# Performance work log

Hardware: AMD Instinct MI355X
Metric: run time of the kernel (lower is better)

## Reference

```python
import jax, jax.numpy as jnp
import numpy as np

VOCAB, EMBED, HIDDEN, NCLS, PAD = 50257, 512, 1024, 2, 0

def setup_inputs() -> dict:
    key = jax.random.key(0)
    ks = jax.random.split(key, 16)
    def xavier(k, shape):
        fan_in, fan_out = shape[1], shape[0]
        lim = jnp.sqrt(6.0 / (fan_in + fan_out))
        return jax.random.uniform(k, shape, jnp.float32, -lim, lim)
    x = jax.random.randint(ks[0], (64, 512), 0, VOCAB, dtype=jnp.int32)
    emb = jax.random.uniform(ks[1], (VOCAB, EMBED), jnp.float32, -0.1, 0.1)
    emb = emb.at[PAD].set(0.0)
    return {
        'x': x,
        'emb': emb,
        'W_ii': xavier(ks[2], (HIDDEN, EMBED)), 'b_ii': jnp.zeros((HIDDEN,), jnp.float32),
        'W_hi': xavier(ks[3], (HIDDEN, HIDDEN)),
        'W_if': xavier(ks[4], (HIDDEN, EMBED)), 'b_if': jnp.zeros((HIDDEN,), jnp.float32),
        'W_hf': xavier(ks[5], (HIDDEN, HIDDEN)),
        'W_ig': xavier(ks[6], (HIDDEN, EMBED)), 'b_ig': jnp.zeros((HIDDEN,), jnp.float32),
        'W_hg': xavier(ks[7], (HIDDEN, HIDDEN)),
        'W_io': xavier(ks[8], (HIDDEN, EMBED)), 'b_io': jnp.zeros((HIDDEN,), jnp.float32),
        'W_ho': xavier(ks[9], (HIDDEN, HIDDEN)),
        'V_w': xavier(ks[10], (NCLS, HIDDEN)), 'V_b': jnp.zeros((NCLS,), jnp.float32),
    }


def _lstm_forward(x, emb, W_ii, b_ii, W_hi, W_if, b_if, W_hf, W_ig, b_ig, W_hg, W_io, b_io, W_ho, V_w, V_b):
    # Dropout layers act as identity in eval mode.
    e = emb[x]  # [B,S,E]
    B, S, E = e.shape
    H = W_hi.shape[0]
    # Precompute all input-to-gate projections in one batched GEMM.
    Wx = jnp.stack([W_ii, W_if, W_ig, W_io], axis=0)      # [4,H,E]
    bx = jnp.stack([b_ii, b_if, b_ig, b_io], axis=0)      # [4,H]
    gates_x = jnp.einsum('bse,ghe->sbgh', e, Wx) + bx     # [S,B,4,H]
    Wh = jnp.stack([W_hi, W_hf, W_hg, W_ho], axis=0)      # [4,H,H]

    def step(carry, gx):
        h, c = carry
        gh = jnp.einsum('bk,ghk->bgh', h, Wh)             # [B,4,H]
        g = gx + gh
        i_t = jax.nn.sigmoid(g[:, 0])
        f_t = jax.nn.sigmoid(g[:, 1])
        g_t = jnp.tanh(g[:, 2])
        o_t = jax.nn.sigmoid(g[:, 3])
        c = f_t * c + i_t * g_t
        h = o_t * jnp.tanh(c)
        return (h, c), None

    h0 = jnp.zeros((B, H), e.dtype)
    c0 = jnp.zeros((B, H), e.dtype)
    (h, c), _ = jax.lax.scan(step, (h0, c0), gates_x)
    out = h @ V_w.T + V_b
    return out, (h, c)


def reference(x, emb, W_ii, b_ii, W_hi, W_if, b_if, W_hf, W_ig, b_ig, W_hg, W_io, b_io, W_ho, V_w, V_b):
    return _lstm_forward(x, emb, W_ii, b_ii, W_hi, W_if, b_if, W_hf, W_ig, b_ig, W_hg, W_io, b_io, W_ho, V_w, V_b)
```

## Files before the change

### kernel.cpp

```cpp
#include <hip/hip_runtime.h>
#include <math.h>

#define Bn 64
#define Hn 1024
#define En 512
#define Sn 512
#define RING 32
#define NBLK 256

typedef _Float16 f16;
typedef _Float16 half8 __attribute__((ext_vector_type(8)));
typedef float f32x4 __attribute__((ext_vector_type(4)));
typedef unsigned long long u64;
typedef u64 u64x2 __attribute__((ext_vector_type(2)));


__global__ __launch_bounds__(256) void wpack_kernel(
    const float* __restrict__ Whi_, const float* __restrict__ Whf_,
    const float* __restrict__ Whg_, const float* __restrict__ Who_,
    const float* __restrict__ Wxi_, const float* __restrict__ Wxf_,
    const float* __restrict__ Wxg_, const float* __restrict__ Wxo_,
    f16* __restrict__ wpHi, f16* __restrict__ wpLo)
{
    int t = blockIdx.x * 256 + threadIdx.x;
    int lane = t & 63;
    int rest = t >> 6;
    int kc = rest % 48;
    int bb = rest / 48;
    int n = lane & 15, g = n >> 2, du = n & 3;
    int u = bb * 4 + du;
    int klo = (lane >> 4) << 3;
    const float* Wh = (g == 0 ? Whi_ : g == 1 ? Whf_ : g == 2 ? Whg_ : Who_);
    const float* Wx = (g == 0 ? Wxi_ : g == 1 ? Wxf_ : g == 2 ? Wxg_ : Wxo_);
    const float* src = (kc < 32) ? (Wh + (size_t)u * Hn + kc * 32 + klo)
                                 : (Wx + (size_t)u * En + (kc - 32) * 32 + klo);
    float4 v0 = ((const float4*)src)[0];
    float4 v1 = ((const float4*)src)[1];
    float w[8] = {v0.x, v0.y, v0.z, v0.w, v1.x, v1.y, v1.z, v1.w};
    #pragma unroll
    for (int j = 0; j < 8; ++j) {
        f16 hi = (f16)w[j];
        float lo = (w[j] - (float)hi) * 2048.0f;
        wpHi[(size_t)t * 8 + j] = hi;
        wpLo[(size_t)t * 8 + j] = (f16)lo;
    }
}

__global__ __launch_bounds__(256) void epack_kernel(
    const int* __restrict__ x, const float* __restrict__ emb,
    f16* __restrict__ eF)
{
    int t = blockIdx.x * 256 + threadIdx.x;
    int lane = t & 63;
    int q = t >> 6;
    int mt = q & 3; q >>= 2;
    int kc2 = q & 15;
    int s = q >> 4;
    int b = mt * 16 + (lane & 15);
    int tok = x[b * Sn + s];
    int k = kc2 * 32 + ((lane >> 4) << 3);
    const float* src = emb + (size_t)tok * En + k;
    float4 v0 = ((const float4*)src)[0];
    float4 v1 = ((const float4*)src)[1];
    f16* dst = eF + (size_t)t * 8;
    dst[0] = (f16)v0.x; dst[1] = (f16)v0.y; dst[2] = (f16)v0.z; dst[3] = (f16)v0.w;
    dst[4] = (f16)v1.x; dst[5] = (f16)v1.y; dst[6] = (f16)v1.z; dst[7] = (f16)v1.w;
}

__global__ __launch_bounds__(256) void gx_chunk_kernel(
    const half8* __restrict__ eF,
    const half8* __restrict__ wpHi, const half8* __restrict__ wpLo,
    float* __restrict__ gx, int chunk)
{
    int lane = threadIdx.x & 63;
    int id = blockIdx.x * 4 + (threadIdx.x >> 6);
    int sc = id >> 8;
    int bb = id & 255;
    int s = chunk * RING + sc;

    const half8* eFs = eF + (size_t)s * 4096 + lane;
    const half8* bH = wpHi + ((size_t)(bb * 48 + 32)) * 64 + lane;
    const half8* bL = wpLo + ((size_t)(bb * 48 + 32)) * 64 + lane;

    f32x4 aH[4], aL[4];
    #pragma unroll
    for (int mt = 0; mt < 4; ++mt) { aH[mt] = (f32x4)0.0f; aL[mt] = (f32x4)0.0f; }

    for (int kcx = 0; kcx < 16; ++kcx) {
        half8 bh = bH[(size_t)kcx * 64];
        half8 bl = bL[(size_t)kcx * 64];
        #pragma unroll
        for (int mt = 0; mt < 4; ++mt) {
            half8 a = eFs[(size_t)((kcx * 4 + mt) * 64)];
            aH[mt] = __builtin_amdgcn_mfma_f32_16x16x32_f16(a, bh, aH[mt], 0, 0, 0);
            aL[mt] = __builtin_amdgcn_mfma_f32_16x16x32_f16(a, bl, aL[mt], 0, 0, 0);
        }
    }

    int n = lane & 15, g = n >> 2, du = n & 3;
    int col = (g << 10) + bb * 4 + du;
    float* g0 = gx + (size_t)sc * (Bn * 4096) + col;
    #pragma unroll
    for (int mt = 0; mt < 4; ++mt) {
        #pragma unroll
        for (int r = 0; r < 4; ++r) {
            int b = mt * 16 + ((lane >> 4) << 2) + r;
            g0[(size_t)b * 4096] = aH[mt][r] + aL[mt][r] * (1.0f / 2048.0f);
        }
    }
}

template<bool USE_GX>
__global__ __launch_bounds__(1024) void step_kernel(
    const f16* __restrict__ hFin, f16* __restrict__ hFout,
    const half8* __restrict__ eF,
    const half8* __restrict__ wpHi, const half8* __restrict__ wpLo,
    const float* __restrict__ gx,
    const float* __restrict__ bi, const float* __restrict__ bf,
    const float* __restrict__ bg, const float* __restrict__ bo,
    float* __restrict__ c, float* __restrict__ hFinal, int s)
{
    __shared__ float preW[16][256];

    const int tid  = threadIdx.x;
    const int lane = tid & 63;
    const int wv   = tid >> 6;
    const int mt   = wv & 3;
    const int kq   = wv >> 2;
    const int bb   = blockIdx.x;

    const half8* hin = (const half8*)hFin + lane;
    const half8* bHb = wpHi + (size_t)(bb * 48) * 64 + lane;
    const half8* bLb = wpLo + (size_t)(bb * 48) * 64 + lane;

    f32x4 accH = {0.f, 0.f, 0.f, 0.f};
    f32x4 accL = {0.f, 0.f, 0.f, 0.f};

    if (USE_GX) {
        #pragma unroll
        for (int i = 0; i < 8; ++i) {
            int kc = kq * 8 + i;
            half8 a  = hin[(size_t)((kc * 4 + mt) * 64)];
            half8 bh = bHb[(size_t)kc * 64];
            half8 bl = bLb[(size_t)kc * 64];
            accH = __builtin_amdgcn_mfma_f32_16x16x32_f16(a, bh, accH, 0, 0, 0);
            accL = __builtin_amdgcn_mfma_f32_16x16x32_f16(a, bl, accL, 0, 0, 0);
        }
    } else {
        const half8* eFs = eF + (size_t)s * 4096 + lane;
        #pragma unroll
        for (int i = 0; i < 12; ++i) {
            int kc = kq * 12 + i;
            half8 a = (kc < 32) ? hin[(size_t)((kc * 4 + mt) * 64)]
                                : eFs[(size_t)(((kc - 32) * 4 + mt) * 64)];
            half8 bh = bHb[(size_t)kc * 64];
            half8 bl = bLb[(size_t)kc * 64];
            accH = __builtin_amdgcn_mfma_f32_16x16x32_f16(a, bh, accH, 0, 0, 0);
            accL = __builtin_amdgcn_mfma_f32_16x16x32_f16(a, bl, accL, 0, 0, 0);
        }
    }

    f32x4 v;
    #pragma unroll
    for (int r = 0; r < 4; ++r) v[r] = accH[r] + accL[r] * (1.0f / 2048.0f);
    *(f32x4*)&preW[wv][lane * 4] = v;
    __syncthreads();

    if (tid < 256) {
        const int bcell = tid >> 2, ducell = tid & 3;
        const int colcell = bb * 4 + ducell;
        const int msub = bcell & 15, mtp = bcell >> 4;
        const int base_i = ((msub >> 2) * 16) * 4 + (msub & 3);
        float sg_[4];
        #pragma unroll
        for (int g = 0; g < 4; ++g) {
            int idx = base_i + (g * 4 + ducell) * 4;
            sg_[g] = preW[0 * 4 + mtp][idx] + preW[1 * 4 + mtp][idx]
                   + preW[2 * 4 + mtp][idx] + preW[3 * 4 + mtp][idx];
        }
        float si = sg_[0] + bi[colcell];
        float sf = sg_[1] + bf[colcell];
        float sg = sg_[2] + bg[colcell];
        float so = sg_[3] + bo[colcell];
        if (USE_GX) {
            const float* gr = gx + ((size_t)(s & (RING - 1)) * Bn + bcell) * 4096;
            si += gr[colcell];        sf += gr[1024 + colcell];
            sg += gr[2048 + colcell]; so += gr[3072 + colcell];
        }
        float it = 1.f / (1.f + expf(-si));
        float ft = 1.f / (1.f + expf(-sf));
        float gt = tanhf(sg);
        float ot = 1.f / (1.f + expf(-so));
        int gi = bcell * Hn + colcell;
        float cn = ft * c[gi] + it * gt;
        c[gi] = cn;
        float hn = ot * tanhf(cn);
        int kch = colcell >> 5, dk = colcell & 31;
        int lp  = ((dk >> 3) << 4) | (bcell & 15);
        int mtp2 = bcell >> 4;
        hFout[((size_t)((kch * 4 + mtp2) * 64 + lp)) * 8 + (dk & 7)] = (f16)hn;
        if (s == Sn - 1) hFinal[gi] = hn;
    }
}

__global__ __launch_bounds__(1024) void steps_chunk_coop(
    f16* __restrict__ hF,
    const half8* __restrict__ eF,
    const half8* __restrict__ wpHi, const half8* __restrict__ wpLo,
    float* __restrict__ gx,
    const float* __restrict__ bi, const float* __restrict__ bf,
    const float* __restrict__ bg, const float* __restrict__ bo,
    float* __restrict__ c, float* __restrict__ hFinal,
    unsigned* __restrict__ cntArr, int chunk)
{
    __shared__ alignas(16) f16 wHs[32 * 512];
    __shared__ alignas(16) f16 wLs[32 * 512];
    __shared__ float preW[16][256];

    const int tid  = threadIdx.x;
    const int lane = tid & 63;
    const int wv   = tid >> 6;
    const int mt   = wv & 3;
    const int kq   = wv >> 2;
    const int bb   = blockIdx.x;

    {
        const half8* srcH = wpHi + (size_t)(bb * 48) * 64;
        const half8* srcL = wpLo + (size_t)(bb * 48) * 64;
        half8* dH = (half8*)wHs;
        half8* dL = (half8*)wLs;
        #pragma unroll
        for (int i = 0; i < 2; ++i) {
            dH[tid + i * 1024] = srcH[tid + i * 1024];
            dL[tid + i * 1024] = srcL[tid + i * 1024];
        }
    }

    {
        const half8* bH = wpHi + ((size_t)(bb * 48 + 32)) * 64 + lane;
        const half8* bL = wpLo + ((size_t)(bb * 48 + 32)) * 64 + lane;
        #pragma unroll
        for (int t2 = 0; t2 < 2; ++t2) {
            int sc = wv * 2 + t2;
            int s = chunk * RING + sc;
            const half8* eFs = eF + (size_t)s * 4096 + lane;
            f32x4 aH[4], aL[4];
            #pragma unroll
            for (int m2 = 0; m2 < 4; ++m2) { aH[m2] = (f32x4)0.0f; aL[m2] = (f32x4)0.0f; }
            for (int kcx = 0; kcx < 16; ++kcx) {
                half8 bh = bH[(size_t)kcx * 64];
                half8 bl = bL[(size_t)kcx * 64];
                #pragma unroll
                for (int m2 = 0; m2 < 4; ++m2) {
                    half8 a = eFs[(size_t)((kcx * 4 + m2) * 64)];
                    aH[m2] = __builtin_amdgcn_mfma_f32_16x16x32_f16(a, bh, aH[m2], 0, 0, 0);
                    aL[m2] = __builtin_amdgcn_mfma_f32_16x16x32_f16(a, bl, aL[m2], 0, 0, 0);
                }
            }
            int n = lane & 15, g = n >> 2, du = n & 3;
            int col = (g << 10) + bb * 4 + du;
            float* g0 = gx + (size_t)sc * (Bn * 4096) + col;
            #pragma unroll
            for (int m2 = 0; m2 < 4; ++m2) {
                #pragma unroll
                for (int r = 0; r < 4; ++r) {
                    int b = m2 * 16 + ((lane >> 4) << 2) + r;
                    g0[(size_t)b * 4096] = aH[m2][r] + aL[m2][r] * (1.0f / 2048.0f);
                }
            }
        }
    }

    float creg = 0.f, bi_r = 0.f, bf_r = 0.f, bg_r = 0.f, bo_r = 0.f;
    int bcell = 0, ducell = 0, colcell = 0, gi = 0, mtp = 0, base_i = 0;
    int kch = 0, dk = 0, lp = 0;
    if (tid < 256) {
        bcell = tid >> 2; ducell = tid & 3;
        colcell = bb * 4 + ducell;
        gi = bcell * Hn + colcell;
        int msub = bcell & 15; mtp = bcell >> 4;
        base_i = ((msub >> 2) * 16) * 4 + (msub & 3);
        creg = c[gi];
        bi_r = bi[colcell]; bf_r = bf[colcell];
        bg_r = bg[colcell]; bo_r = bo[colcell];
        kch = colcell >> 5; dk = colcell & 31;
        lp  = ((dk >> 3) << 4) | (bcell & 15);
    }

    __syncthreads();

    const half8* wHl = (const half8*)wHs + lane;
    const half8* wLl = (const half8*)wLs + lane;

    #pragma unroll 1
    for (int sc = 0; sc < RING; ++sc) {
        const int s = chunk * RING + sc;
        const f16* hbase = hF + (size_t)(s & 1) * 65536;
        f16* hout = hF + (size_t)((s + 1) & 1) * 65536;

        float gxi = 0.f, gxf = 0.f, gxg = 0.f, gxo = 0.f;
        if (tid < 256) {
            const float* gr = gx + ((size_t)sc * Bn + bcell) * 4096 + colcell;
            gxi = gr[0];    gxf = gr[1024];
            gxg = gr[2048]; gxo = gr[3072];
        }

        half8 afr[8];
        #pragma unroll
        for (int i = 0; i < 8; ++i) {
            const int kc = kq * 8 + i;
            const u64* p = (const u64*)(hbase
                + ((size_t)((kc * 4 + mt) * 64 + lane)) * 8);
            u64x2 u;
            u.x = __hip_atomic_load(p, __ATOMIC_RELAXED,
                                    __HIP_MEMORY_SCOPE_AGENT);
            u.y = __hip_atomic_load(p + 1, __ATOMIC_RELAXED,
                                    __HIP_MEMORY_SCOPE_AGENT);
            afr[i] = __builtin_bit_cast(half8, u);
        }

        f32x4 accH = {0.f, 0.f, 0.f, 0.f};
        f32x4 accL = {0.f, 0.f, 0.f, 0.f};
        #pragma unroll
        for (int i = 0; i < 8; ++i) {
            const int kc = kq * 8 + i;
            half8 bh = wHl[(size_t)kc * 64];
            half8 bl = wLl[(size_t)kc * 64];
            accH = __builtin_amdgcn_mfma_f32_16x16x32_f16(afr[i], bh, accH, 0, 0, 0);
            accL = __builtin_amdgcn_mfma_f32_16x16x32_f16(afr[i], bl, accL, 0, 0, 0);
        }
        f32x4 v;
        #pragma unroll
        for (int r = 0; r < 4; ++r) v[r] = accH[r] + accL[r] * (1.0f / 2048.0f);
        *(f32x4*)&preW[wv][lane * 4] = v;
        __syncthreads();

        if (tid < 256) {
            float sg_[4];
            #pragma unroll
            for (int g = 0; g < 4; ++g) {
                int idx = base_i + (g * 4 + ducell) * 4;
                sg_[g] = preW[mtp][idx] + preW[4 + mtp][idx]
                       + preW[8 + mtp][idx] + preW[12 + mtp][idx];
            }
            float si = sg_[0] + bi_r + gxi;
            float sf = sg_[1] + bf_r + gxf;
            float sg = sg_[2] + bg_r + gxg;
            float so = sg_[3] + bo_r + gxo;
            float it = 1.f / (1.f + expf(-si));
            float ft = 1.f / (1.f + expf(-sf));
            float gt = tanhf(sg);
            float ot = 1.f / (1.f + expf(-so));
            float cn = ft * creg + it * gt;
            creg = cn;
            float hn = ot * tanhf(cn);
            union { f16 h; unsigned short u; } cv;
            cv.h = (f16)hn;
            unsigned short* paddr = (unsigned short*)(hout
                + ((size_t)((kch * 4 + mtp) * 64 + lp)) * 8 + (dk & 7));
            __hip_atomic_store(paddr, cv.u, __ATOMIC_RELAXED,
                               __HIP_MEMORY_SCOPE_AGENT);
            if (s == Sn - 1) hFinal[gi] = hn;
        }

        if (sc < RING - 1) {
            asm volatile("s_waitcnt vmcnt(0)" ::: "memory");
            __syncthreads();
            if (tid == 0) {
                const unsigned B = (unsigned)(chunk * (RING - 1) + sc);
                unsigned old = __hip_atomic_fetch_add(
                    cntArr + ((unsigned)(bb & 15) << 5), 1u,
                    __ATOMIC_RELAXED, __HIP_MEMORY_SCOPE_AGENT);
                if ((old & 15u) == 15u) {
                    unsigned m = __hip_atomic_fetch_add(
                        cntArr + 512, 1u,
                        __ATOMIC_RELAXED, __HIP_MEMORY_SCOPE_AGENT);
                    if (m == 16u * B + 15u)
                        __hip_atomic_store(cntArr + 544, B + 1u,
                            __ATOMIC_RELAXED, __HIP_MEMORY_SCOPE_AGENT);
                }
                while (__hip_atomic_load(cntArr + 544, __ATOMIC_RELAXED,
                                         __HIP_MEMORY_SCOPE_AGENT) < B + 1u)
                    __builtin_amdgcn_s_sleep(1);
            }
            __syncthreads();
        }
    }

    if (tid < 256) c[gi] = creg;
}

__global__ __launch_bounds__(256) void copy_hc(
    const float* __restrict__ h, const float* __restrict__ c,
    float* __restrict__ out)
{
    int i = blockIdx.x * 256 + threadIdx.x;
    out[128 + i] = h[i];
    out[128 + Bn * Hn + i] = c[i];
}

__global__ __launch_bounds__(64) void classifier(
    const float* __restrict__ h, const float* __restrict__ Vw,
    const float* __restrict__ Vb, float* __restrict__ out)
{
    int bid = blockIdx.x;
    int b = bid >> 1, n = bid & 1;
    int lane = threadIdx.x;
    float sum = 0.f;
    for (int k = lane; k < Hn; k += 64)
        sum += h[b * Hn + k] * Vw[n * Hn + k];
    #pragma unroll
    for (int off = 32; off > 0; off >>= 1)
        sum += __shfl_down(sum, off, 64);
    if (lane == 0)
        out[b * 2 + n] = sum + Vb[n];
}


#define KT 128
#define KTP 132

__global__ __launch_bounds__(256) void lstm_step_fb(
    const int* __restrict__ x, const float* __restrict__ emb,
    const float* __restrict__ Wxi, const float* __restrict__ Wxf,
    const float* __restrict__ Wxg, const float* __restrict__ Wxo,
    const float* __restrict__ bi, const float* __restrict__ bf,
    const float* __restrict__ bg, const float* __restrict__ bo,
    const float* __restrict__ Whi, const float* __restrict__ Whf,
    const float* __restrict__ Whg, const float* __restrict__ Who,
    const float* __restrict__ h_in, const float* __restrict__ c_in,
    float* __restrict__ h_out, float* __restrict__ c_out, int s)
{
    __shared__ float sh[Bn][KTP];
    __shared__ float sw[16][KTP];
    const int tid = threadIdx.x;
    const int b = tid >> 2, j = tid & 3;
    const int cb = blockIdx.x * 4, col = cb + j;
    float acc0 = 0.f, acc1 = 0.f, acc2 = 0.f, acc3 = 0.f;

    for (int k0 = 0; k0 < En; k0 += KT) {
        for (int i = tid; i < Bn * (KT / 4); i += 256) {
            int bl = i >> 5, k4 = (i & 31) << 2;
            int tok = x[bl * Sn + s];
            *reinterpret_cast<float4*>(&sh[bl][k4]) =
                *reinterpret_cast<const float4*>(&emb[(size_t)tok * En + k0 + k4]);
        }
        for (int i = tid; i < 16 * (KT / 4); i += 256) {
            int r = i >> 5, k4 = (i & 31) << 2;
            const float* Wg = (r < 8) ? ((r < 4) ? Wxi : Wxf)
                                      : ((r < 12) ? Wxg : Wxo);
            *reinterpret_cast<float4*>(&sw[r][k4]) =
                *reinterpret_cast<const float4*>(&Wg[(size_t)(cb + (r & 3)) * En + k0 + k4]);
        }
        __syncthreads();
        #pragma unroll 8
        for (int k = 0; k < KT; k += 4) {
            float4 hv = *reinterpret_cast<const float4*>(&sh[b][k]);
            float4 w0 = *reinterpret_cast<const float4*>(&sw[j][k]);
            float4 w1 = *reinterpret_cast<const float4*>(&sw[4 + j][k]);
            float4 w2 = *reinterpret_cast<const float4*>(&sw[8 + j][k]);
            float4 w3 = *reinterpret_cast<const float4*>(&sw[12 + j][k]);
            acc0 += hv.x*w0.x + hv.y*w0.y + hv.z*w0.z + hv.w*w0.w;
            acc1 += hv.x*w1.x + hv.y*w1.y + hv.z*w1.z + hv.w*w1.w;
            acc2 += hv.x*w2.x + hv.y*w2.y + hv.z*w2.z + hv.w*w2.w;
            acc3 += hv.x*w3.x + hv.y*w3.y + hv.z*w3.z + hv.w*w3.w;
        }
        __syncthreads();
    }
    for (int k0 = 0; k0 < Hn; k0 += KT) {
        for (int i = tid; i < Bn * (KT / 4); i += 256) {
            int bl = i >> 5, k4 = (i & 31) << 2;
            *reinterpret_cast<float4*>(&sh[bl][k4]) =
                *reinterpret_cast<const float4*>(&h_in[(size_t)bl * Hn + k0 + k4]);
        }
        for (int i = tid; i < 16 * (KT / 4); i += 256) {
            int r = i >> 5, k4 = (i & 31) << 2;
            const float* Wg = (r < 8) ? ((r < 4) ? Whi : Whf)
                                      : ((r < 12) ? Whg : Who);
            *reinterpret_cast<float4*>(&sw[r][k4]) =
                *reinterpret_cast<const float4*>(&Wg[(size_t)(cb + (r & 3)) * Hn + k0 + k4]);
        }
        __syncthreads();
        #pragma unroll 8
        for (int k = 0; k < KT; k += 4) {
            float4 hv = *reinterpret_cast<const float4*>(&sh[b][k]);
            float4 w0 = *reinterpret_cast<const float4*>(&sw[j][k]);
            float4 w1 = *reinterpret_cast<const float4*>(&sw[4 + j][k]);
            float4 w2 = *reinterpret_cast<const float4*>(&sw[8 + j][k]);
            float4 w3 = *reinterpret_cast<const float4*>(&sw[12 + j][k]);
            acc0 += hv.x*w0.x + hv.y*w0.y + hv.z*w0.z + hv.w*w0.w;
            acc1 += hv.x*w1.x + hv.y*w1.y + hv.z*w1.z + hv.w*w1.w;
            acc2 += hv.x*w2.x + hv.y*w2.y + hv.z*w2.z + hv.w*w2.w;
            acc3 += hv.x*w3.x + hv.y*w3.y + hv.z*w3.z + hv.w*w3.w;
        }
        __syncthreads();
    }
    acc0 += bi[col]; acc1 += bf[col]; acc2 += bg[col]; acc3 += bo[col];
    float it = 1.f / (1.f + expf(-acc0));
    float ft = 1.f / (1.f + expf(-acc1));
    float gt = tanhf(acc2);
    float ot = 1.f / (1.f + expf(-acc3));
    float cn = ft * c_in[b * Hn + col] + it * gt;
    c_out[b * Hn + col] = cn;
    h_out[b * Hn + col] = ot * tanhf(cn);
}


extern "C" void kernel_launch(void* const* d_in, const int* in_sizes, int n_in,
                              void* d_out, int out_size, void* d_ws, size_t ws_size,
                              hipStream_t stream) {
    const int*   x   = (const int*)  d_in[0];
    const float* emb = (const float*)d_in[1];
    const float* Wxi = (const float*)d_in[2];
    const float* bi  = (const float*)d_in[3];
    const float* Whi = (const float*)d_in[4];
    const float* Wxf = (const float*)d_in[5];
    const float* bf  = (const float*)d_in[6];
    const float* Whf = (const float*)d_in[7];
    const float* Wxg = (const float*)d_in[8];
    const float* bg  = (const float*)d_in[9];
    const float* Whg = (const float*)d_in[10];
    const float* Wxo = (const float*)d_in[11];
    const float* bo  = (const float*)d_in[12];
    const float* Who = (const float*)d_in[13];
    const float* Vw  = (const float*)d_in[14];
    const float* Vb  = (const float*)d_in[15];
    float* out = (float*)d_out;

    const size_t szHF = (size_t)2 * 65536 * sizeof(f16);
    const size_t szC  = (size_t)Bn * Hn * sizeof(float);
    const size_t szEF = (size_t)Sn * 16 * 4 * 64 * 8 * sizeof(f16);
    const size_t szWp = (size_t)256 * 48 * 64 * 8 * sizeof(f16);
    const size_t szGx = (size_t)RING * Bn * 4096 * sizeof(float);
    const size_t need_mid  = szHF + 2 * szC + szEF + 2 * szWp;
    const size_t need_gx   = need_mid + szGx;
    const size_t need_coop = need_gx + 4096;

    if (ws_size >= need_mid) {
        const bool haveGx   = (ws_size >= need_gx);
        const bool haveCoop = (ws_size >= need_coop);
        char* base = (char*)d_ws;
        f16*   hF   = (f16*)base;   base += szHF;
        float* c    = (float*)base; base += szC;
        float* h    = (float*)base; base += szC;
        f16*   eF   = (f16*)base;   base += szEF;
        f16*   wpHi = (f16*)base;   base += szWp;
        f16*   wpLo = (f16*)base;   base += szWp;
        float* gx   = (float*)base; base += szGx;
        unsigned* cnt = (unsigned*)base;

        hipMemsetAsync(d_ws, 0, szHF + szC, stream);
        if (haveCoop) hipMemsetAsync(cnt, 0, 4096, stream);
        wpack_kernel<<<dim3(3072), dim3(256), 0, stream>>>(
            Whi, Whf, Whg, Who, Wxi, Wxf, Wxg, Wxo, wpHi, wpLo);
        epack_kernel<<<dim3(8192), dim3(256), 0, stream>>>(x, emb, eF);

        if (haveGx) {
            bool coop = haveCoop;
            for (int chunk = 0; chunk < Sn / RING; ++chunk) {
                if (coop) {
                    f16* hFp = hF;
                    const half8* eF8   = (const half8*)eF;
                    const half8* wpHi8 = (const half8*)wpHi;
                    const half8* wpLo8 = (const half8*)wpLo;
                    float* gxp = gx;
                    const float* bip = bi; const float* bfp = bf;
                    const float* bgp = bg; const float* bop = bo;
                    float* cp = c; float* hp = h;
                    unsigned* cntp = cnt;
                    int ci = chunk;
                    void* args[] = { &hFp, &eF8, &wpHi8, &wpLo8, &gxp,
                                     &bip, &bfp, &bgp, &bop, &cp, &hp,
                                     &cntp, &ci };
                    hipError_t e = hipLaunchCooperativeKernel(
                        (const void*)steps_chunk_coop, dim3(NBLK), dim3(1024),
                        args, 0, stream);
                    if (e != hipSuccess) { coop = false; (void)hipGetLastError(); }
                }
                if (!coop) {
                    gx_chunk_kernel<<<dim3(2048), dim3(256), 0, stream>>>(
                        (const half8*)eF, (const half8*)wpHi, (const half8*)wpLo,
                        gx, chunk);
                    for (int sc = 0; sc < RING; ++sc) {
                        int s = chunk * RING + sc;
                        const f16* hin  = hF + (size_t)(s & 1) * 65536;
                        f16*       hout = hF + (size_t)((s + 1) & 1) * 65536;
                        step_kernel<true><<<dim3(256), dim3(1024), 0, stream>>>(
                            hin, hout, (const half8*)eF,
                            (const half8*)wpHi, (const half8*)wpLo,
                            gx, bi, bf, bg, bo, c, h, s);
                    }
                }
            }
        } else {
            for (int s = 0; s < Sn; ++s) {
                const f16* hin  = hF + (size_t)(s & 1) * 65536;
                f16*       hout = hF + (size_t)((s + 1) & 1) * 65536;
                step_kernel<false><<<dim3(256), dim3(1024), 0, stream>>>(
                    hin, hout, (const half8*)eF,
                    (const half8*)wpHi, (const half8*)wpLo,
                    (const float*)nullptr, bi, bf, bg, bo, c, h, s);
            }
        }
        copy_hc<<<dim3(Bn * Hn / 256), dim3(256), 0, stream>>>(h, c, out);
        classifier<<<dim3(Bn * 2), dim3(64), 0, stream>>>(h, Vw, Vb, out);
    } else {
        float* hA = (float*)d_ws;
        float* cA = hA + Bn * Hn;
        float* hB = cA + Bn * Hn;
        float* cB = hB + Bn * Hn;
        hipMemsetAsync(d_ws, 0, (size_t)2 * Bn * Hn * sizeof(float), stream);
        for (int s = 0; s < Sn; ++s) {
            const float* hi = (s & 1) ? hB : hA;
            const float* ci = (s & 1) ? cB : cA;
            float* ho = (s & 1) ? hA : hB;
            float* co = (s & 1) ? cA : cB;
            lstm_step_fb<<<dim3(Hn / 4), dim3(256), 0, stream>>>(
                x, emb, Wxi, Wxf, Wxg, Wxo, bi, bf, bg, bo,
                Whi, Whf, Whg, Who, hi, ci, ho, co, s);
        }
        copy_hc<<<dim3(Bn * Hn / 256), dim3(256), 0, stream>>>(hA, cA, out);
        classifier<<<dim3(Bn * 2), dim3(64), 0, stream>>>(hA, Vw, Vb, out);
    }
}
```

Measured before the change: 4.579 ms.

## Flatten grid barrier, pack h stores into 64-bit writes, prefetch gate inputs

```diff
diff --git a/kernel.cpp b/kernel.cpp
--- a/kernel.cpp
+++ b/kernel.cpp
@@ -292,18 +292,18 @@
     const half8* wHl = (const half8*)wHs + lane;
     const half8* wLl = (const half8*)wLs + lane;
 
+    float gxi = 0.f, gxf = 0.f, gxg = 0.f, gxo = 0.f;
+    if (tid < 256) {
+        const float* gr = gx + ((size_t)0 * Bn + bcell) * 4096 + colcell;
+        gxi = gr[0];    gxf = gr[1024];
+        gxg = gr[2048]; gxo = gr[3072];
+    }
+
     #pragma unroll 1
     for (int sc = 0; sc < RING; ++sc) {
         const int s = chunk * RING + sc;
         const f16* hbase = hF + (size_t)(s & 1) * 65536;
         f16* hout = hF + (size_t)((s + 1) & 1) * 65536;
-
-        float gxi = 0.f, gxf = 0.f, gxg = 0.f, gxo = 0.f;
-        if (tid < 256) {
-            const float* gr = gx + ((size_t)sc * Bn + bcell) * 4096 + colcell;
-            gxi = gr[0];    gxf = gr[1024];
-            gxg = gr[2048]; gxo = gr[3072];
-        }
 
         half8 afr[8];
         #pragma unroll
@@ -356,32 +356,47 @@
             float hn = ot * tanhf(cn);
             union { f16 h; unsigned short u; } cv;
             cv.h = (f16)hn;
-            unsigned short* paddr = (unsigned short*)(hout
-                + ((size_t)((kch * 4 + mtp) * 64 + lp)) * 8 + (dk & 7));
-            __hip_atomic_store(paddr, cv.u, __ATOMIC_RELAXED,
-                               __HIP_MEMORY_SCOPE_AGENT);
+            unsigned v0 = cv.u;
+            unsigned v1 = (unsigned)__shfl_down((int)v0, 1, 64);
+            unsigned v2 = (unsigned)__shfl_down((int)v0, 2, 64);
+            unsigned v3 = (unsigned)__shfl_down((int)v0, 3, 64);
+            if (ducell == 0) {
+                u64 pack = (u64)(v0 & 0xffffu) | ((u64)(v1 & 0xffffu) << 16)
+                         | ((u64)(v2 & 0xffffu) << 32) | ((u64)(v3 & 0xffffu) << 48);
+                u64* paddr = (u64*)(hout
+                    + ((size_t)((kch * 4 + mtp) * 64 + lp)) * 8 + (dk & 7));
+                __hip_atomic_store(paddr, pack, __ATOMIC_RELAXED,
+                                   __HIP_MEMORY_SCOPE_AGENT);
+            }
             if (s == Sn - 1) hFinal[gi] = hn;
         }
 
         if (sc < RING - 1) {
             asm volatile("s_waitcnt vmcnt(0)" ::: "memory");
             __syncthreads();
-            if (tid == 0) {
+            if (tid == 0)
+                __hip_atomic_fetch_add(cntArr + (((unsigned)bb & 15u) << 5), 1u,
+                                       __ATOMIC_RELAXED, __HIP_MEMORY_SCOPE_AGENT);
+            if (tid < 256) {
+                const float* gr = gx + ((size_t)(sc + 1) * Bn + bcell) * 4096
+                                + colcell;
+                gxi = gr[0];    gxf = gr[1024];
+                gxg = gr[2048]; gxo = gr[3072];
+            }
+            if (wv == 0) {
                 const unsigned B = (unsigned)(chunk * (RING - 1) + sc);
-                unsigned old = __hip_atomic_fetch_add(
-                    cntArr + ((unsigned)(bb & 15) << 5), 1u,
-                    __ATOMIC_RELAXED, __HIP_MEMORY_SCOPE_AGENT);
-                if ((old & 15u) == 15u) {
-                    unsigned m = __hip_atomic_fetch_add(
-                        cntArr + 512, 1u,
+                const unsigned need = 256u * (B + 1u);
+                while (true) {
+                    unsigned pv = __hip_atomic_load(
+                        cntArr + (((unsigned)lane & 15u) << 5),
                         __ATOMIC_RELAXED, __HIP_MEMORY_SCOPE_AGENT);
-                    if (m == 16u * B + 15u)
-                        __hip_atomic_store(cntArr + 544, B + 1u,
-                            __ATOMIC_RELAXED, __HIP_MEMORY_SCOPE_AGENT);
+                    pv += (unsigned)__shfl_xor((int)pv, 1, 64);
+                    pv += (unsigned)__shfl_xor((int)pv, 2, 64);
+                    pv += (unsigned)__shfl_xor((int)pv, 4, 64);
+                    pv += (unsigned)__shfl_xor((int)pv, 8, 64);
+                    if (pv >= need) break;
+                    __builtin_amdgcn_s_sleep(1);
                 }
-                while (__hip_atomic_load(cntArr + 544, __ATOMIC_RELAXED,
-                                         __HIP_MEMORY_SCOPE_AGENT) < B + 1u)
-                    __builtin_amdgcn_s_sleep(1);
             }
             __syncthreads();
         }
```

New measurement: 4.256 ms. -7.1%, faster.
